# Kernel tuning notes

Measured on AMD Instinct MI355X. Metric: run time of the kernel, lower is better.

Reference implementation:

```python
import jax, jax.numpy as jnp
import numpy as np
import math

B, NTOK, NH, D = 8, 1000, 8, 64
CHUNK = 8  # query-chunk size for the pairwise L1 score computation


def _linearm(w, x):
    # LinearM: w [out, in+1] (last column is bias); x [b, t, in] -> [b, t, out]
    return jnp.einsum('oi,bti->bto', w[:, :-1], x) + w[:, -1]


def setup_inputs() -> dict:
    key = jax.random.key(0)
    ks = jax.random.split(key, 4)
    scl = 0.005
    x = jax.random.normal(ks[0], (B, NTOK, D), dtype=jnp.float32)
    wq = (scl * jax.random.normal(ks[1], (NH * D, D + 1), dtype=jnp.float32)).at[:, -1].set(0.0)
    wv = (scl * jax.random.normal(ks[2], (NH * D, D + 1), dtype=jnp.float32)).at[:, -1].set(0.0)
    wk = scl * jnp.ones((NH, D), dtype=jnp.float32)
    wf = (scl * jax.random.normal(ks[3], (D, D + 1), dtype=jnp.float32)).at[:, -1].set(0.0)
    return {"x": x, "wq": wq, "wv": wv, "wk": wk, "wf": wf}


def _forward(x, wq, wv, wk, wf):
    b, t, d = x.shape
    nh = wk.shape[0]
    scale = 1.0 / math.sqrt(d)

    q = _linearm(wq, x).reshape(b, t, nh, d)          # [b, t, nh, d]
    v = _linearm(wv, x).reshape(b, t, nh, d)          # [b, t, nh, d]
    k = x[:, :, None, :] * wk[None, None]             # [b, t, nh, d]

    # L1-distance attention scores: a[b, s, q, h] = -scale * sum_w |q[b,q,h,w] - k[b,s,h,w]|
    # Computed in query chunks so the [b, t, t, nh, d] pairwise tensor is never materialized.
    nc = t // CHUNK
    qc = q.reshape(b, nc, CHUNK, nh, d).transpose(1, 0, 2, 3, 4)  # [nc, b, C, nh, d]

    @jax.checkpoint
    def scores(qch):
        # qch: [b, C, nh, d] -> [b, t(src), C, nh]
        return -scale * jnp.sum(jnp.abs(qch[:, None] - k[:, :, None]), axis=-1)

    a = jax.lax.map(scores, qc)                       # [nc, b, t, C, nh]
    a = a.transpose(1, 2, 0, 3, 4).reshape(b, t, t, nh)  # [b, src, dst, nh]

    # Extra all-zero "null" source row (mirrors a[:, a2len, :, :] = 0 before softmax)
    a = jnp.concatenate([a, jnp.zeros((b, 1, t, nh), a.dtype)], axis=1)
    a = jax.nn.softmax(a, axis=1)[:, :t]              # softmax over sources, drop null row

    # einsum('bsdh,bshw->bdhw') followed by sum over heads, fused:
    out = jnp.einsum('bsth,bshw->btw', a, v)          # [b, t, d]

    y = jax.nn.relu(out)                              # self.gelu is actually ReLU
    y = _linearm(wf, y)
    return x + y


def reference(x, wq, wv, wk, wf):
    return _forward(x, wq, wv, wk, wf)
```

## Files before the change

kernel.cpp:

```cpp
#include <hip/hip_runtime.h>
#include <math.h>

#define Bb 8
#define Tt 1000
#define TPAD 1024
#define NHh 8
#define Dd 64

typedef short bf16x8 __attribute__((ext_vector_type(8)));
typedef float f32x4 __attribute__((ext_vector_type(4)));

#define QOFF (-0.3f)
#define QSTEP (0.6f / 256.0f)
#define QINV (256.0f / 0.6f)
#define CQ (-0.125f * 1.44269504088896341f * QSTEP)

__device__ __forceinline__ unsigned sad_u8(unsigned a, unsigned b, unsigned c) {
#if __has_builtin(__builtin_amdgcn_sad_u8)
    return __builtin_amdgcn_sad_u8(a, b, c);
#else
    unsigned d;
    asm("v_sad_u8 %0, %1, %2, %3" : "=v"(d) : "v"(a), "v"(b), "v"(c));
    return d;
#endif
}

__device__ __forceinline__ unsigned quant8(float v) {
    float t = (v - QOFF) * QINV + 0.5f;
    t = fminf(fmaxf(t, 0.0f), 255.0f);
    return (unsigned)(int)t;
}

__device__ __forceinline__ unsigned cvt_pk_bf16(float lo, float hi) {
    unsigned r;
    asm("v_cvt_pk_bf16_f32 %0, %1, %2" : "=v"(r) : "v"(lo), "v"(hi));
    return r;
}

__device__ __forceinline__ bf16x8 mkbf(unsigned u0, unsigned u1, unsigned u2, unsigned u3) {
    union { unsigned u[4]; bf16x8 v; } x;
    x.u[0] = u0; x.u[1] = u1; x.u[2] = u2; x.u[3] = u3;
    return x.v;
}

__device__ __forceinline__ bf16x8 bfc(uint4 q) {
    union { uint4 q; bf16x8 v; } x; x.q = q; return x.v;
}

__global__ __launch_bounds__(256) void prep_kernel(
    const float* __restrict__ x, const float* __restrict__ wq,
    const float* __restrict__ wv, const float* __restrict__ wk,
    unsigned* __restrict__ qq8, unsigned* __restrict__ kq8,
    uint4* __restrict__ vfrag)
{
    __shared__ float xs[64][68];
    __shared__ float ws[64][65];
    __shared__ float vS[64][68];
    const int tid = threadIdx.x;
    const int st = blockIdx.x;
    const int cb = blockIdx.y;
    const int b  = blockIdx.z;
    const bool isQ = (cb < 8);
    const int h = isQ ? cb : (cb - 8);
    const float* W = isQ ? wq : wv;
    const int cBase = h * 64;
    const int bh = b * NHh + h;

#pragma unroll
    for (int i = 0; i < 4; ++i) {
        int f4 = tid + i * 256;
        int r = f4 >> 4, c4 = (f4 & 15) << 2;
        int row = st * 64 + r; if (row >= Tt) row = Tt - 1;
        *(float4*)&xs[r][c4] = *(const float4*)&x[((size_t)b * Tt + row) * 64 + c4];
    }
#pragma unroll
    for (int i = 0; i < 16; ++i) {
        int idx = tid + i * 256;
        int c = idx >> 6, k = idx & 63;
        ws[c][k] = W[(cBase + c) * 65 + k];
    }
    __syncthreads();

    const int rg = tid >> 4, cg = tid & 15;
    const int r0 = rg * 4, c0 = cg * 4;
    float acc[4][4];
#pragma unroll
    for (int j = 0; j < 4; ++j) {
        float bias = W[(cBase + c0 + j) * 65 + 64];
#pragma unroll
        for (int i = 0; i < 4; ++i) acc[i][j] = bias;
    }
    for (int k0 = 0; k0 < 64; k0 += 4) {
        float4 a[4];
#pragma unroll
        for (int i = 0; i < 4; ++i) a[i] = *(const float4*)&xs[r0 + i][k0];
#pragma unroll
        for (int j = 0; j < 4; ++j) {
            float b0 = ws[c0 + j][k0 + 0];
            float b1 = ws[c0 + j][k0 + 1];
            float b2 = ws[c0 + j][k0 + 2];
            float b3 = ws[c0 + j][k0 + 3];
#pragma unroll
            for (int i = 0; i < 4; ++i)
                acc[i][j] += a[i].x * b0 + a[i].y * b1 + a[i].z * b2 + a[i].w * b3;
        }
    }

    if (isQ) {
#pragma unroll
        for (int i = 0; i < 4; ++i) {
            int t = st * 64 + r0 + i;
            unsigned d = 0u;
            if (t < Tt)
                d = quant8(acc[i][0]) | (quant8(acc[i][1]) << 8) |
                    (quant8(acc[i][2]) << 16) | (quant8(acc[i][3]) << 24);
            qq8[((size_t)bh * TPAD + t) * 16 + cg] = d;
        }
        {
            const int r = tid >> 2, c4 = tid & 3;
            const int t = st * 64 + r;
            unsigned kd[4];
            if (t < Tt) {
#pragma unroll
                for (int dw = 0; dw < 4; ++dw) {
                    int w = c4 * 16 + dw * 4;
                    float4 wkv = *(const float4*)&wk[h * 64 + w];
                    kd[dw] = quant8(xs[r][w + 0] * wkv.x) |
                             (quant8(xs[r][w + 1] * wkv.y) << 8) |
                             (quant8(xs[r][w + 2] * wkv.z) << 16) |
                             (quant8(xs[r][w + 3] * wkv.w) << 24);
                }
            } else {
                kd[0] = kd[1] = kd[2] = kd[3] = 0u;
            }
            *(uint4*)&kq8[((size_t)bh * TPAD + t) * 16 + c4 * 4] =
                make_uint4(kd[0], kd[1], kd[2], kd[3]);
        }
    } else {
#pragma unroll
        for (int i = 0; i < 4; ++i) {
            float4 o; o.x = acc[i][0]; o.y = acc[i][1]; o.z = acc[i][2]; o.w = acc[i][3];
            *(float4*)&vS[r0 + i][c0] = o;
        }
        __syncthreads();
#pragma unroll
        for (int e2 = 0; e2 < 2; ++e2) {
            int ent = tid + e2 * 256;
            int kk = ent >> 8, rem = ent & 255, n = rem >> 6, lane = rem & 63;
            int ts = kk * 32 + ((lane >> 4) << 3);
            int w  = n * 16 + (lane & 15);
            unsigned o[4];
#pragma unroll
            for (int pr = 0; pr < 4; ++pr) {
                int t0 = st * 64 + ts + pr * 2;
                float lo = (t0 < Tt)     ? vS[ts + pr * 2][w]     : 0.0f;
                float hi = (t0 + 1 < Tt) ? vS[ts + pr * 2 + 1][w] : 0.0f;
                o[pr] = cvt_pk_bf16(lo, hi);
            }
            vfrag[(((size_t)bh * 16 + st) * 8 + (kk * 4 + n)) * 64 + lane] =
                make_uint4(o[0], o[1], o[2], o[3]);
        }
    }
}

__global__ __launch_bounds__(256) void attn_kernel(
    const unsigned* __restrict__ qq8, const unsigned* __restrict__ kq8,
    const uint4* __restrict__ vfrag, float* __restrict__ part)
{
    __shared__ unsigned kS[2][1024];
    __shared__ uint4    vS[2][512];

    const int tid = threadIdx.x;
    const int wv_ = tid >> 6;
    const int l   = tid & 63;
    const int g   = l >> 4;
    const int m   = l & 15;
    const int qt  = blockIdx.x;
    const int h   = blockIdx.y, b = blockIdx.z;
    const int bh  = b * NHh + h;

    unsigned qv[16];
    {
        const uint4* qp = (const uint4*)(qq8 + ((size_t)bh * TPAD + qt * 64 + wv_ * 16 + m) * 16);
        *(uint4*)&qv[0]  = qp[0];
        *(uint4*)&qv[4]  = qp[1];
        *(uint4*)&qv[8]  = qp[2];
        *(uint4*)&qv[12] = qp[3];
    }

    const uint4* kg = (const uint4*)(kq8 + (size_t)bh * TPAD * 16);
    const uint4* vg = vfrag + (size_t)bh * (16 * 512);

    const int krow = tid >> 2, kc = tid & 3;
    const int kdst = (krow << 2) + (kc ^ ((krow >> 3) & 3));

    {
        uint4 k0 = kg[tid];
        uint4 v0 = vg[tid];
        uint4 v1 = vg[256 + tid];
        *(uint4*)&kS[0][kdst << 2] = k0;
        vS[0][tid] = v0;
        vS[0][256 + tid] = v1;
    }
    __syncthreads();

    f32x4 acc0 = {0.f,0.f,0.f,0.f}, acc1 = acc0, acc2 = acc0, acc3 = acc0;
    float dsum = 0.0f;

#pragma unroll 1
    for (int t = 0; t < 16; ++t) {
        const int cur = t & 1;

        const int tn = (t < 15) ? t + 1 : 15;
        uint4 kn  = kg[tn * 256 + tid];
        uint4 vn0 = vg[tn * 512 + tid];
        uint4 vn1 = vg[tn * 512 + 256 + tid];

        bf16x8 A0, A1;
#pragma unroll
        for (int kk = 0; kk < 2; ++kk) {
            unsigned accu[8];
#pragma unroll
            for (int e = 0; e < 8; ++e) {
                const unsigned* kb = &kS[cur][(kk * 32 + (g << 3) + e) << 4];
                uint4 c0 = *(const uint4*)(kb + ((0 ^ g) << 2));
                uint4 c1 = *(const uint4*)(kb + ((1 ^ g) << 2));
                uint4 c2 = *(const uint4*)(kb + ((2 ^ g) << 2));
                uint4 c3 = *(const uint4*)(kb + ((3 ^ g) << 2));
                const unsigned* k0 = (const unsigned*)&c0;
                const unsigned* k1 = (const unsigned*)&c1;
                const unsigned* k2 = (const unsigned*)&c2;
                const unsigned* k3 = (const unsigned*)&c3;
                unsigned sa = 0u, sb = 0u;
#pragma unroll
                for (int w = 0; w < 4; ++w) sa = sad_u8(qv[w],      k0[w], sa);
#pragma unroll
                for (int w = 0; w < 4; ++w) sb = sad_u8(qv[4 + w],  k1[w], sb);
#pragma unroll
                for (int w = 0; w < 4; ++w) sa = sad_u8(qv[8 + w],  k2[w], sa);
#pragma unroll
                for (int w = 0; w < 4; ++w) sb = sad_u8(qv[12 + w], k3[w], sb);
                accu[e] = sa + sb;
            }
            const bool maskall = (t == 15) && (kk == 1) && (g >= 1);
            float p[8];
#pragma unroll
            for (int e = 0; e < 8; ++e) {
                p[e] = maskall ? 0.0f : __builtin_amdgcn_exp2f(CQ * (float)accu[e]);
                dsum += p[e];
            }
            bf16x8 A = mkbf(cvt_pk_bf16(p[0], p[1]), cvt_pk_bf16(p[2], p[3]),
                            cvt_pk_bf16(p[4], p[5]), cvt_pk_bf16(p[6], p[7]));
            if (kk == 0) A0 = A; else A1 = A;
        }

        {
            uint4 vf0 = vS[cur][0 * 64 + l], vf1 = vS[cur][1 * 64 + l];
            uint4 vf2 = vS[cur][2 * 64 + l], vf3 = vS[cur][3 * 64 + l];
            acc0 = __builtin_amdgcn_mfma_f32_16x16x32_bf16(A0, bfc(vf0), acc0, 0, 0, 0);
            acc1 = __builtin_amdgcn_mfma_f32_16x16x32_bf16(A0, bfc(vf1), acc1, 0, 0, 0);
            acc2 = __builtin_amdgcn_mfma_f32_16x16x32_bf16(A0, bfc(vf2), acc2, 0, 0, 0);
            acc3 = __builtin_amdgcn_mfma_f32_16x16x32_bf16(A0, bfc(vf3), acc3, 0, 0, 0);
        }
        {
            uint4 vf4 = vS[cur][4 * 64 + l], vf5 = vS[cur][5 * 64 + l];
            uint4 vf6 = vS[cur][6 * 64 + l], vf7 = vS[cur][7 * 64 + l];
            acc0 = __builtin_amdgcn_mfma_f32_16x16x32_bf16(A1, bfc(vf4), acc0, 0, 0, 0);
            acc1 = __builtin_amdgcn_mfma_f32_16x16x32_bf16(A1, bfc(vf5), acc1, 0, 0, 0);
            acc2 = __builtin_amdgcn_mfma_f32_16x16x32_bf16(A1, bfc(vf6), acc2, 0, 0, 0);
            acc3 = __builtin_amdgcn_mfma_f32_16x16x32_bf16(A1, bfc(vf7), acc3, 0, 0, 0);
        }

        if (t < 15) {
            *(uint4*)&kS[cur ^ 1][kdst << 2] = kn;
            vS[cur ^ 1][tid] = vn0;
            vS[cur ^ 1][256 + tid] = vn1;
        }
        __syncthreads();
    }

    dsum += __shfl_xor(dsum, 16);
    dsum += __shfl_xor(dsum, 32);
    const float den = 1.0f + dsum;

#pragma unroll
    for (int j = 0; j < 4; ++j) {
        float dj = __shfl(den, g * 4 + j);
        int row = qt * 64 + wv_ * 16 + g * 4 + j;
        if (row < Tt) {
            float inv = 1.0f / dj;
            float* o = part + (((size_t)b * Tt + row) * NHh + h) * 64 + m;
            o[0]  = acc0[j] * inv;
            o[16] = acc1[j] * inv;
            o[32] = acc2[j] * inv;
            o[48] = acc3[j] * inv;
        }
    }
}

__global__ __launch_bounds__(256) void finalize_kernel(
    const float* __restrict__ x, const float* __restrict__ wf,
    const float* __restrict__ part, float* __restrict__ out)
{
    __shared__ float wfs[64][65];
    __shared__ float osh[4][64];
    const int tid = threadIdx.x;
    for (int i = tid; i < 64 * 65; i += 256) wfs[i / 65][i % 65] = wf[i];
    const int wave = tid >> 6, lane = tid & 63;
    const int token = blockIdx.x * 4 + wave;
    float o = 0.f;
    const float* pt = part + (size_t)token * NHh * Dd;
#pragma unroll
    for (int hh = 0; hh < NHh; ++hh) o += pt[hh * Dd + lane];
    o = fmaxf(o, 0.f);
    osh[wave][lane] = o;
    __syncthreads();
    float acc = wfs[lane][64];
#pragma unroll 8
    for (int w = 0; w < 64; ++w) acc += wfs[lane][w] * osh[wave][w];
    out[(size_t)token * Dd + lane] = x[(size_t)token * Dd + lane] + acc;
}

extern "C" void kernel_launch(void* const* d_in, const int* in_sizes, int n_in,
                              void* d_out, int out_size, void* d_ws, size_t ws_size,
                              hipStream_t stream)
{
    const float* x  = (const float*)d_in[0];
    const float* wq = (const float*)d_in[1];
    const float* wv = (const float*)d_in[2];
    const float* wk = (const float*)d_in[3];
    const float* wf = (const float*)d_in[4];
    float* out = (float*)d_out;

    char* base = (char*)d_ws;
    float*    part  = (float*)base;
    unsigned* qq8   = (unsigned*)(base + 16384000);
    unsigned* kq8   = (unsigned*)(base + 16384000 + 4194304);
    uint4*    vfrag = (uint4*)(base + 16384000 + 2 * 4194304);

    prep_kernel<<<dim3(16, 16, Bb), 256, 0, stream>>>(x, wq, wv, wk, qq8, kq8, vfrag);
    attn_kernel<<<dim3(16, NHh, Bb), 256, 0, stream>>>(qq8, kq8, vfrag, part);
    finalize_kernel<<<2000, 256, 0, stream>>>(x, wf, part, out);
}
```

Before: 95.80 us.

## Process two query row-tiles per wave and stage K/V via direct global-to-LDS loads

The attention kernel now runs 128 threads per block, and each wave handles 32 query rows instead of 16. Every K and V fragment read from LDS is therefore reused for two query tiles in the SAD and MFMA work, which halves LDS traffic per unit of compute. K/V tiles are copied with global_load_lds straight into shared memory, and the K swizzle moves into prep_kernel's store layout so no register round trip is needed. The cost is higher register pressure from doubled accumulators and query registers, and half as many waves per block, which can lower occupancy and latency hiding.

```diff
diff --git a/kernel.cpp b/kernel.cpp
--- a/kernel.cpp
+++ b/kernel.cpp
@@ -46,6 +46,10 @@
 __device__ __forceinline__ bf16x8 bfc(uint4 q) {
     union { uint4 q; bf16x8 v; } x; x.q = q; return x.v;
 }
+
+#define GLDS(gsrc, ldst) \
+    __builtin_amdgcn_global_load_lds((const __attribute__((address_space(1))) unsigned*)(gsrc), \
+                                     (__attribute__((address_space(3))) unsigned*)(ldst), 16, 0, 0)
 
 __global__ __launch_bounds__(256) void prep_kernel(
     const float* __restrict__ x, const float* __restrict__ wq,
@@ -133,7 +137,8 @@
             } else {
                 kd[0] = kd[1] = kd[2] = kd[3] = 0u;
             }
-            *(uint4*)&kq8[((size_t)bh * TPAD + t) * 16 + c4 * 4] =
+            const int c4s = c4 ^ ((r >> 3) & 3);
+            *(uint4*)&kq8[((size_t)bh * TPAD + t) * 16 + c4s * 4] =
                 make_uint4(kd[0], kd[1], kd[2], kd[3]);
         }
     } else {
@@ -163,7 +168,7 @@
     }
 }
 
-__global__ __launch_bounds__(256) void attn_kernel(
+__global__ __launch_bounds__(128) void attn_kernel(
     const unsigned* __restrict__ qq8, const unsigned* __restrict__ kq8,
     const uint4* __restrict__ vfrag, float* __restrict__ part)
 {
@@ -178,48 +183,56 @@
     const int qt  = blockIdx.x;
     const int h   = blockIdx.y, b = blockIdx.z;
     const int bh  = b * NHh + h;
-
-    unsigned qv[16];
+    const int rowbase = qt * 64 + wv_ * 32;
+
+    unsigned qa[16], qb[16];
     {
-        const uint4* qp = (const uint4*)(qq8 + ((size_t)bh * TPAD + qt * 64 + wv_ * 16 + m) * 16);
-        *(uint4*)&qv[0]  = qp[0];
-        *(uint4*)&qv[4]  = qp[1];
-        *(uint4*)&qv[8]  = qp[2];
-        *(uint4*)&qv[12] = qp[3];
-    }
-
-    const uint4* kg = (const uint4*)(kq8 + (size_t)bh * TPAD * 16);
-    const uint4* vg = vfrag + (size_t)bh * (16 * 512);
-
-    const int krow = tid >> 2, kc = tid & 3;
-    const int kdst = (krow << 2) + (kc ^ ((krow >> 3) & 3));
+        const uint4* qp = (const uint4*)qq8 + ((size_t)bh * TPAD + rowbase + m) * 4;
+        *(uint4*)&qa[0]  = qp[0];  *(uint4*)&qa[4]  = qp[1];
+        *(uint4*)&qa[8]  = qp[2];  *(uint4*)&qa[12] = qp[3];
+        const uint4* qp2 = qp + 16 * 4;
+        *(uint4*)&qb[0]  = qp2[0]; *(uint4*)&qb[4]  = qp2[1];
+        *(uint4*)&qb[8]  = qp2[2]; *(uint4*)&qb[12] = qp2[3];
+    }
+
+    const uint4* kg = (const uint4*)kq8 + (size_t)bh * 4096;
+    const uint4* vg = vfrag + (size_t)bh * 8192;
 
     {
-        uint4 k0 = kg[tid];
-        uint4 v0 = vg[tid];
-        uint4 v1 = vg[256 + tid];
-        *(uint4*)&kS[0][kdst << 2] = k0;
-        vS[0][tid] = v0;
-        vS[0][256 + tid] = v1;
+        const uint4* kt = kg;
+        const uint4* vt = vg;
+        GLDS(kt + wv_ * 64 +   0 + l, &kS[0][(wv_ * 64 +   0) * 4]);
+        GLDS(kt + wv_ * 64 + 128 + l, &kS[0][(wv_ * 64 + 128) * 4]);
+        GLDS(vt + wv_ * 64 +   0 + l, &vS[0][wv_ * 64 +   0]);
+        GLDS(vt + wv_ * 64 + 128 + l, &vS[0][wv_ * 64 + 128]);
+        GLDS(vt + wv_ * 64 + 256 + l, &vS[0][wv_ * 64 + 256]);
+        GLDS(vt + wv_ * 64 + 384 + l, &vS[0][wv_ * 64 + 384]);
     }
     __syncthreads();
 
-    f32x4 acc0 = {0.f,0.f,0.f,0.f}, acc1 = acc0, acc2 = acc0, acc3 = acc0;
-    float dsum = 0.0f;
+    f32x4 aca[4], acb[4];
+#pragma unroll
+    for (int n = 0; n < 4; ++n) { aca[n] = (f32x4){0.f,0.f,0.f,0.f}; acb[n] = aca[n]; }
+    float dsum_a = 0.0f, dsum_b = 0.0f;
 
 #pragma unroll 1
     for (int t = 0; t < 16; ++t) {
         const int cur = t & 1;
 
-        const int tn = (t < 15) ? t + 1 : 15;
-        uint4 kn  = kg[tn * 256 + tid];
-        uint4 vn0 = vg[tn * 512 + tid];
-        uint4 vn1 = vg[tn * 512 + 256 + tid];
-
-        bf16x8 A0, A1;
+        if (t < 15) {
+            const uint4* kt = kg + (t + 1) * 256;
+            const uint4* vt = vg + (t + 1) * 512;
+            GLDS(kt + wv_ * 64 +   0 + l, &kS[cur ^ 1][(wv_ * 64 +   0) * 4]);
+            GLDS(kt + wv_ * 64 + 128 + l, &kS[cur ^ 1][(wv_ * 64 + 128) * 4]);
+            GLDS(vt + wv_ * 64 +   0 + l, &vS[cur ^ 1][wv_ * 64 +   0]);
+            GLDS(vt + wv_ * 64 + 128 + l, &vS[cur ^ 1][wv_ * 64 + 128]);
+            GLDS(vt + wv_ * 64 + 256 + l, &vS[cur ^ 1][wv_ * 64 + 256]);
+            GLDS(vt + wv_ * 64 + 384 + l, &vS[cur ^ 1][wv_ * 64 + 384]);
+        }
+
 #pragma unroll
         for (int kk = 0; kk < 2; ++kk) {
-            unsigned accu[8];
+            unsigned ca[8], cb[8];
 #pragma unroll
             for (int e = 0; e < 8; ++e) {
                 const unsigned* kb = &kS[cur][(kk * 32 + (g << 3) + e) << 4];
@@ -231,69 +244,84 @@
                 const unsigned* k1 = (const unsigned*)&c1;
                 const unsigned* k2 = (const unsigned*)&c2;
                 const unsigned* k3 = (const unsigned*)&c3;
-                unsigned sa = 0u, sb = 0u;
-#pragma unroll
-                for (int w = 0; w < 4; ++w) sa = sad_u8(qv[w],      k0[w], sa);
-#pragma unroll
-                for (int w = 0; w < 4; ++w) sb = sad_u8(qv[4 + w],  k1[w], sb);
-#pragma unroll
-                for (int w = 0; w < 4; ++w) sa = sad_u8(qv[8 + w],  k2[w], sa);
-#pragma unroll
-                for (int w = 0; w < 4; ++w) sb = sad_u8(qv[12 + w], k3[w], sb);
-                accu[e] = sa + sb;
+                unsigned sa0 = 0u, sa1 = 0u, sb0 = 0u, sb1 = 0u;
+#pragma unroll
+                for (int w = 0; w < 4; ++w) {
+                    sa0 = sad_u8(qa[w],      k0[w], sa0);
+                    sa1 = sad_u8(qa[4 + w],  k1[w], sa1);
+                    sb0 = sad_u8(qb[w],      k0[w], sb0);
+                    sb1 = sad_u8(qb[4 + w],  k1[w], sb1);
+                }
+#pragma unroll
+                for (int w = 0; w < 4; ++w) {
+                    sa0 = sad_u8(qa[8 + w],  k2[w], sa0);
+                    sa1 = sad_u8(qa[12 + w], k3[w], sa1);
+                    sb0 = sad_u8(qb[8 + w],  k2[w], sb0);
+                    sb1 = sad_u8(qb[12 + w], k3[w], sb1);
+                }
+                ca[e] = sa0 + sa1;
+                cb[e] = sb0 + sb1;
             }
+
             const bool maskall = (t == 15) && (kk == 1) && (g >= 1);
-            float p[8];
+            float pa[8], pb[8];
 #pragma unroll
             for (int e = 0; e < 8; ++e) {
-                p[e] = maskall ? 0.0f : __builtin_amdgcn_exp2f(CQ * (float)accu[e]);
-                dsum += p[e];
+                pa[e] = maskall ? 0.0f : __builtin_amdgcn_exp2f(CQ * (float)ca[e]);
+                pb[e] = maskall ? 0.0f : __builtin_amdgcn_exp2f(CQ * (float)cb[e]);
+                dsum_a += pa[e];
+                dsum_b += pb[e];
             }
-            bf16x8 A = mkbf(cvt_pk_bf16(p[0], p[1]), cvt_pk_bf16(p[2], p[3]),
-                            cvt_pk_bf16(p[4], p[5]), cvt_pk_bf16(p[6], p[7]));
-            if (kk == 0) A0 = A; else A1 = A;
-        }
-
-        {
-            uint4 vf0 = vS[cur][0 * 64 + l], vf1 = vS[cur][1 * 64 + l];
-            uint4 vf2 = vS[cur][2 * 64 + l], vf3 = vS[cur][3 * 64 + l];
-            acc0 = __builtin_amdgcn_mfma_f32_16x16x32_bf16(A0, bfc(vf0), acc0, 0, 0, 0);
-            acc1 = __builtin_amdgcn_mfma_f32_16x16x32_bf16(A0, bfc(vf1), acc1, 0, 0, 0);
-            acc2 = __builtin_amdgcn_mfma_f32_16x16x32_bf16(A0, bfc(vf2), acc2, 0, 0, 0);
-            acc3 = __builtin_amdgcn_mfma_f32_16x16x32_bf16(A0, bfc(vf3), acc3, 0, 0, 0);
-        }
-        {
-            uint4 vf4 = vS[cur][4 * 64 + l], vf5 = vS[cur][5 * 64 + l];
-            uint4 vf6 = vS[cur][6 * 64 + l], vf7 = vS[cur][7 * 64 + l];
-            acc0 = __builtin_amdgcn_mfma_f32_16x16x32_bf16(A1, bfc(vf4), acc0, 0, 0, 0);
-            acc1 = __builtin_amdgcn_mfma_f32_16x16x32_bf16(A1, bfc(vf5), acc1, 0, 0, 0);
-            acc2 = __builtin_amdgcn_mfma_f32_16x16x32_bf16(A1, bfc(vf6), acc2, 0, 0, 0);
-            acc3 = __builtin_amdgcn_mfma_f32_16x16x32_bf16(A1, bfc(vf7), acc3, 0, 0, 0);
-        }
-
-        if (t < 15) {
-            *(uint4*)&kS[cur ^ 1][kdst << 2] = kn;
-            vS[cur ^ 1][tid] = vn0;
-            vS[cur ^ 1][256 + tid] = vn1;
-        }
+            bf16x8 Aa = mkbf(cvt_pk_bf16(pa[0], pa[1]), cvt_pk_bf16(pa[2], pa[3]),
+                             cvt_pk_bf16(pa[4], pa[5]), cvt_pk_bf16(pa[6], pa[7]));
+            bf16x8 Ab = mkbf(cvt_pk_bf16(pb[0], pb[1]), cvt_pk_bf16(pb[2], pb[3]),
+                             cvt_pk_bf16(pb[4], pb[5]), cvt_pk_bf16(pb[6], pb[7]));
+
+            uint4 vf0 = vS[cur][(kk * 4 + 0) * 64 + l];
+            uint4 vf1 = vS[cur][(kk * 4 + 1) * 64 + l];
+            uint4 vf2 = vS[cur][(kk * 4 + 2) * 64 + l];
+            uint4 vf3 = vS[cur][(kk * 4 + 3) * 64 + l];
+            aca[0] = __builtin_amdgcn_mfma_f32_16x16x32_bf16(Aa, bfc(vf0), aca[0], 0, 0, 0);
+            acb[0] = __builtin_amdgcn_mfma_f32_16x16x32_bf16(Ab, bfc(vf0), acb[0], 0, 0, 0);
+            aca[1] = __builtin_amdgcn_mfma_f32_16x16x32_bf16(Aa, bfc(vf1), aca[1], 0, 0, 0);
+            acb[1] = __builtin_amdgcn_mfma_f32_16x16x32_bf16(Ab, bfc(vf1), acb[1], 0, 0, 0);
+            aca[2] = __builtin_amdgcn_mfma_f32_16x16x32_bf16(Aa, bfc(vf2), aca[2], 0, 0, 0);
+            acb[2] = __builtin_amdgcn_mfma_f32_16x16x32_bf16(Ab, bfc(vf2), acb[2], 0, 0, 0);
+            aca[3] = __builtin_amdgcn_mfma_f32_16x16x32_bf16(Aa, bfc(vf3), aca[3], 0, 0, 0);
+            acb[3] = __builtin_amdgcn_mfma_f32_16x16x32_bf16(Ab, bfc(vf3), acb[3], 0, 0, 0);
+        }
+
         __syncthreads();
     }
 
-    dsum += __shfl_xor(dsum, 16);
-    dsum += __shfl_xor(dsum, 32);
-    const float den = 1.0f + dsum;
+    dsum_a += __shfl_xor(dsum_a, 16);
+    dsum_a += __shfl_xor(dsum_a, 32);
+    dsum_b += __shfl_xor(dsum_b, 16);
+    dsum_b += __shfl_xor(dsum_b, 32);
+    const float den_a = 1.0f + dsum_a;
+    const float den_b = 1.0f + dsum_b;
 
 #pragma unroll
     for (int j = 0; j < 4; ++j) {
-        float dj = __shfl(den, g * 4 + j);
-        int row = qt * 64 + wv_ * 16 + g * 4 + j;
-        if (row < Tt) {
-            float inv = 1.0f / dj;
-            float* o = part + (((size_t)b * Tt + row) * NHh + h) * 64 + m;
-            o[0]  = acc0[j] * inv;
-            o[16] = acc1[j] * inv;
-            o[32] = acc2[j] * inv;
-            o[48] = acc3[j] * inv;
+        float dja = __shfl(den_a, g * 4 + j);
+        float djb = __shfl(den_b, g * 4 + j);
+        int row_a = rowbase + g * 4 + j;
+        int row_b = rowbase + 16 + g * 4 + j;
+        if (row_a < Tt) {
+            float inv = 1.0f / dja;
+            float* o = part + (((size_t)b * Tt + row_a) * NHh + h) * 64 + m;
+            o[0]  = aca[0][j] * inv;
+            o[16] = aca[1][j] * inv;
+            o[32] = aca[2][j] * inv;
+            o[48] = aca[3][j] * inv;
+        }
+        if (row_b < Tt) {
+            float inv = 1.0f / djb;
+            float* o = part + (((size_t)b * Tt + row_b) * NHh + h) * 64 + m;
+            o[0]  = acb[0][j] * inv;
+            o[16] = acb[1][j] * inv;
+            o[32] = acb[2][j] * inv;
+            o[48] = acb[3][j] * inv;
         }
     }
 }
@@ -339,6 +367,6 @@
     uint4*    vfrag = (uint4*)(base + 16384000 + 2 * 4194304);
 
     prep_kernel<<<dim3(16, 16, Bb), 256, 0, stream>>>(x, wq, wv, wk, qq8, kq8, vfrag);
-    attn_kernel<<<dim3(16, NHh, Bb), 256, 0, stream>>>(qq8, kq8, vfrag, part);
+    attn_kernel<<<dim3(16, NHh, Bb), 128, 0, stream>>>(qq8, kq8, vfrag, part);
     finalize_kernel<<<2000, 256, 0, stream>>>(x, wf, part, out);
 }
```

Measured after the change: 100.8 us. +5.2%, slower.

## Use direct global-to-LDS loads with triple-buffered K/V staging in attention

Applied to the files above, without the earlier changes.

Replaces register-staged K/V tile loads with global_load_lds direct-to-LDS transfers. The ring grows from two to three buffers so loads are issued two tiles ahead, synchronised with vmcnt waits and raw barriers. The K swizzle moves into the prep kernel's global write layout, since direct LDS loads cannot permute. This drops the per-thread register round trip and LDS store instructions and hides more load latency, at the cost of more LDS per block, which may reduce occupancy.

```diff
diff --git a/kernel.cpp b/kernel.cpp
--- a/kernel.cpp
+++ b/kernel.cpp
@@ -46,6 +46,10 @@
 __device__ __forceinline__ bf16x8 bfc(uint4 q) {
     union { uint4 q; bf16x8 v; } x; x.q = q; return x.v;
 }
+
+#define GLDS(gsrc, ldst) \
+    __builtin_amdgcn_global_load_lds((const __attribute__((address_space(1))) unsigned*)(gsrc), \
+                                     (__attribute__((address_space(3))) unsigned*)(ldst), 16, 0, 0)
 
 __global__ __launch_bounds__(256) void prep_kernel(
     const float* __restrict__ x, const float* __restrict__ wq,
@@ -133,7 +137,8 @@
             } else {
                 kd[0] = kd[1] = kd[2] = kd[3] = 0u;
             }
-            *(uint4*)&kq8[((size_t)bh * TPAD + t) * 16 + c4 * 4] =
+            const int c4s = c4 ^ ((r >> 3) & 3);
+            *(uint4*)&kq8[((size_t)bh * TPAD + t) * 16 + c4s * 4] =
                 make_uint4(kd[0], kd[1], kd[2], kd[3]);
         }
     } else {
@@ -167,8 +172,8 @@
     const unsigned* __restrict__ qq8, const unsigned* __restrict__ kq8,
     const uint4* __restrict__ vfrag, float* __restrict__ part)
 {
-    __shared__ unsigned kS[2][1024];
-    __shared__ uint4    vS[2][512];
+    __shared__ unsigned kS[3][1024];
+    __shared__ uint4    vS[3][512];
 
     const int tid = threadIdx.x;
     const int wv_ = tid >> 6;
@@ -188,33 +193,30 @@
         *(uint4*)&qv[12] = qp[3];
     }
 
-    const uint4* kg = (const uint4*)(kq8 + (size_t)bh * TPAD * 16);
-    const uint4* vg = vfrag + (size_t)bh * (16 * 512);
-
-    const int krow = tid >> 2, kc = tid & 3;
-    const int kdst = (krow << 2) + (kc ^ ((krow >> 3) & 3));
-
-    {
-        uint4 k0 = kg[tid];
-        uint4 v0 = vg[tid];
-        uint4 v1 = vg[256 + tid];
-        *(uint4*)&kS[0][kdst << 2] = k0;
-        vS[0][tid] = v0;
-        vS[0][256 + tid] = v1;
-    }
-    __syncthreads();
+    const uint4* kg = (const uint4*)kq8 + (size_t)bh * 4096;
+    const uint4* vg = vfrag + (size_t)bh * 8192;
+
+#define STAGE(TT, SB) do { \
+        const uint4* kt_ = kg + (TT) * 256; \
+        const uint4* vt_ = vg + (TT) * 512; \
+        GLDS(kt_ + wv_ * 64 + l,       &kS[SB][(wv_ * 64) * 4]); \
+        GLDS(vt_ + wv_ * 128 + l,      &vS[SB][wv_ * 128]); \
+        GLDS(vt_ + wv_ * 128 + 64 + l, &vS[SB][wv_ * 128 + 64]); \
+    } while (0)
+
+    STAGE(0, 0);
+    STAGE(1, 1);
+    asm volatile("s_waitcnt vmcnt(3)" ::: "memory");
+    __builtin_amdgcn_s_barrier();
+    __builtin_amdgcn_sched_barrier(0);
 
     f32x4 acc0 = {0.f,0.f,0.f,0.f}, acc1 = acc0, acc2 = acc0, acc3 = acc0;
     float dsum = 0.0f;
 
+    int cur = 0, stb = 2;
 #pragma unroll 1
     for (int t = 0; t < 16; ++t) {
-        const int cur = t & 1;
-
-        const int tn = (t < 15) ? t + 1 : 15;
-        uint4 kn  = kg[tn * 256 + tid];
-        uint4 vn0 = vg[tn * 512 + tid];
-        uint4 vn1 = vg[tn * 512 + 256 + tid];
+        if (t < 14) STAGE(t + 2, stb);
 
         bf16x8 A0, A1;
 #pragma unroll
@@ -271,13 +273,19 @@
             acc3 = __builtin_amdgcn_mfma_f32_16x16x32_bf16(A1, bfc(vf7), acc3, 0, 0, 0);
         }
 
+        if (t < 14) {
+            asm volatile("s_waitcnt vmcnt(3)" ::: "memory");
+        } else if (t == 14) {
+            asm volatile("s_waitcnt vmcnt(0)" ::: "memory");
+        }
         if (t < 15) {
-            *(uint4*)&kS[cur ^ 1][kdst << 2] = kn;
-            vS[cur ^ 1][tid] = vn0;
-            vS[cur ^ 1][256 + tid] = vn1;
-        }
-        __syncthreads();
-    }
+            __builtin_amdgcn_s_barrier();
+            __builtin_amdgcn_sched_barrier(0);
+        }
+        cur = (cur == 2) ? 0 : cur + 1;
+        stb = (stb == 2) ? 0 : stb + 1;
+    }
+#undef STAGE
 
     dsum += __shfl_xor(dsum, 16);
     dsum += __shfl_xor(dsum, 32);
```

After: 96.46 us. Within noise of the previous version (+0.7%).
